# Kernel tuning notes

Measured on AMD Instinct MI355X. Metric: run time of the kernel, lower is better.

The kernel has to match this reference:

```python
import math
import jax, jax.numpy as jnp
import numpy as np

B, T, C = 2, 2048, 1024
N_HEAD, N_KV_HEAD = 16, 4
HEAD_DIM = C // N_HEAD  # 64

def _rope(x, cos, sin):
    # x: (B, T, H, D); cos/sin: (1, T, 1, D//2)
    d = x.shape[3] // 2
    x1, x2 = x[..., :d], x[..., d:]
    return jnp.concatenate([x1 * cos + x2 * sin, -x1 * sin + x2 * cos], axis=3)

def _rms_norm(x):
    return x * jax.lax.rsqrt(jnp.mean(x * x, axis=-1, keepdims=True) + 1e-06)

def setup_inputs() -> dict:
    key = jax.random.key(0)
    ks = jax.random.split(key, 9)
    x = jax.random.normal(ks[0], (B, T, C), dtype=jnp.float32)
    ve = jax.random.normal(ks[1], (B, T, N_KV_HEAD * HEAD_DIM), dtype=jnp.float32)
    cos = jax.random.uniform(ks[2], (1, T, 1, HEAD_DIM // 2), dtype=jnp.float32)
    sin = jax.random.uniform(ks[3], (1, T, 1, HEAD_DIM // 2), dtype=jnp.float32)
    s = 1.0 / math.sqrt(C)
    Wq = jax.random.normal(ks[4], (C, N_HEAD * HEAD_DIM), dtype=jnp.float32) * s
    Wk = jax.random.normal(ks[5], (C, N_KV_HEAD * HEAD_DIM), dtype=jnp.float32) * s
    Wv = jax.random.normal(ks[6], (C, N_KV_HEAD * HEAD_DIM), dtype=jnp.float32) * s
    Wproj = jax.random.normal(ks[7], (C, C), dtype=jnp.float32) * s
    Wg = jax.random.normal(ks[8], (12, N_KV_HEAD), dtype=jnp.float32) * (1.0 / math.sqrt(12))
    return {"x": x, "ve": ve, "cos": cos, "sin": sin,
            "Wq": Wq, "Wk": Wk, "Wv": Wv, "Wproj": Wproj, "Wg": Wg,
            "window_size": 1024}

def reference(x, ve, cos, sin, Wq, Wk, Wv, Wproj, Wg, window_size):
    Bb, Tt, Cc = x.shape
    q = (x @ Wq).reshape(Bb, Tt, N_HEAD, HEAD_DIM)
    k = (x @ Wk).reshape(Bb, Tt, N_KV_HEAD, HEAD_DIM)
    v = (x @ Wv).reshape(Bb, Tt, N_KV_HEAD, HEAD_DIM)
    # value-embedding gate (has_ve layer)
    vee = ve.reshape(Bb, Tt, N_KV_HEAD, HEAD_DIM)
    gate = 3.0 * jax.nn.sigmoid(x[..., :12] @ Wg)  # (B, T, n_kv_head)
    v = v + gate[..., None] * vee
    q = _rope(q, cos, sin)
    k = _rope(k, cos, sin)
    q = _rms_norm(q) * 1.2
    k = _rms_norm(k) * 1.2
    repeats = N_HEAD // N_KV_HEAD
    k = jnp.repeat(k, repeats, axis=2)
    v = jnp.repeat(v, repeats, axis=2)
    # sliding-window causal mask
    row = jnp.arange(Tt)[:, None]
    col = jnp.arange(Tt)[None, :]
    mask = (row >= col) & (row - col <= window_size)
    bias = jnp.where(mask, 0.0, -1e9)  # (T, T)
    scale = 1.0 / math.sqrt(HEAD_DIM)
    scores = jnp.einsum("bqhd,bkhd->bhqk", q, k) * scale + bias[None, None]
    attn = jax.nn.softmax(scores, axis=-1)
    y = jnp.einsum("bhqk,bkhd->bqhd", attn, v).reshape(Bb, Tt, Cc)
    return y @ Wproj
```

## Files before the change

kernel.cpp:

```cpp
#include <hip/hip_runtime.h>


typedef __bf16 bf16x8 __attribute__((ext_vector_type(8)));
typedef __bf16 bf16x4 __attribute__((ext_vector_type(4)));
typedef float  f32x4  __attribute__((ext_vector_type(4)));

__device__ __forceinline__ void g2l16(const __bf16* gp, __bf16* lp) {
  __builtin_amdgcn_global_load_lds(
      (const __attribute__((address_space(1))) unsigned int*)(const void*)gp,
      (__attribute__((address_space(3))) unsigned int*)(void*)lp, 16, 0, 0);
}

__global__ void prep(const float* __restrict__ x, __bf16* __restrict__ xb,
                     float* __restrict__ gate, const float* __restrict__ Wg,
                     const float* __restrict__ Wq, const float* __restrict__ Wk,
                     const float* __restrict__ Wv, const float* __restrict__ Wp,
                     __bf16* __restrict__ Wt, __bf16* __restrict__ Wpt) {
  __shared__ float tile[32][33];
  int bid = blockIdx.x;
  if (bid < 2048) {
    int i = (bid * 256 + threadIdx.x) * 8;
    float4 a = *(const float4*)(x + i);
    float4 b = *(const float4*)(x + i + 4);
    bf16x8 o;
    o[0] = (__bf16)a.x; o[1] = (__bf16)a.y; o[2] = (__bf16)a.z; o[3] = (__bf16)a.w;
    o[4] = (__bf16)b.x; o[5] = (__bf16)b.y; o[6] = (__bf16)b.z; o[7] = (__bf16)b.w;
    *(bf16x8*)(xb + i) = o;
    if (threadIdx.x < 8) {
      int row = bid * 2 + (threadIdx.x >> 2);
      int kvh = threadIdx.x & 3;
      float dot = 0.f;
      for (int j = 0; j < 12; ++j) dot += x[(size_t)row * 1024 + j] * Wg[j * 4 + kvh];
      gate[row * 4 + kvh] = 3.f / (1.f + expf(-dot));
    }
    return;
  }
  bid -= 2048;
  int z = bid >> 10, r = bid & 1023;
  int bx = r & 31, by = r >> 5;
  const float* in; __bf16* out; int Cc;
  if (z == 0)      { in = Wq; out = Wt;               Cc = 1024; }
  else if (z == 1) { in = Wk; out = Wt + 1024 * 1024; Cc = 256; }
  else if (z == 2) { in = Wv; out = Wt + 1280 * 1024; Cc = 256; }
  else             { in = Wp; out = Wpt;              Cc = 1024; }
  int c0 = bx * 32, r0 = by * 32;
  if (c0 >= Cc) return;
  int tx = threadIdx.x & 31, ty = threadIdx.x >> 5;
  for (int i = ty; i < 32; i += 8) tile[i][tx] = in[(size_t)(r0 + i) * Cc + c0 + tx];
  __syncthreads();
  for (int i = ty; i < 32; i += 8) out[(size_t)(c0 + i) * 1024 + r0 + tx] = (__bf16)tile[tx][i];
}

__global__ __launch_bounds__(256) void gemm_qkv(const __bf16* __restrict__ A,
                                                const __bf16* __restrict__ Bt,
                                                const float* __restrict__ cosp,
                                                const float* __restrict__ sinp,
                                                const float* __restrict__ gate,
                                                const float* __restrict__ ve,
                                                __bf16* __restrict__ Qb,
                                                __bf16* __restrict__ Kb,
                                                __bf16* __restrict__ Vt) {
  const int K = 1024;
  __shared__ __bf16 As[2 * 64 * 32];
  __shared__ __bf16 Bs[2 * 128 * 32];
  int tid = threadIdx.x;
  int m0 = blockIdx.x * 64, n0 = blockIdx.y * 128;
  int w = tid >> 6, lane = tid & 63, quad = lane >> 4, l16 = lane & 15;
  int wm = (w >> 1) * 32, wn = (w & 1) * 64;

  f32x4 zero = {0.f, 0.f, 0.f, 0.f};
  f32x4 acc[2][4];
  for (int i = 0; i < 2; ++i) for (int j = 0; j < 4; ++j) acc[i][j] = zero;

  int rsub = lane >> 2, cc = (lane & 3) * 8;
  const __bf16* gA  = A  + (size_t)(m0 + w * 16 + rsub) * K + cc;
  const __bf16* gB0 = Bt + (size_t)(n0 + (2 * w) * 16 + rsub) * K + cc;
  const __bf16* gB1 = Bt + (size_t)(n0 + (2 * w + 1) * 16 + rsub) * K + cc;
  __bf16* lA0  = &As[w * 512];            __bf16* lA1  = &As[2048 + w * 512];
  __bf16* lB00 = &Bs[(2 * w) * 512];      __bf16* lB01 = &Bs[4096 + (2 * w) * 512];
  __bf16* lB10 = &Bs[(2 * w + 1) * 512];  __bf16* lB11 = &Bs[4096 + (2 * w + 1) * 512];

  for (int k0 = 0; k0 < K; k0 += 64) {
    __syncthreads();
    g2l16(gA + k0, lA0);       g2l16(gA + k0 + 32, lA1);
    g2l16(gB0 + k0, lB00);     g2l16(gB0 + k0 + 32, lB01);
    g2l16(gB1 + k0, lB10);     g2l16(gB1 + k0 + 32, lB11);
    __syncthreads();
    for (int ks = 0; ks < 2; ++ks) {
      bf16x8 af[2], bfr[4];
      for (int i = 0; i < 2; ++i)
        af[i] = *(const bf16x8*)(&As[ks * 2048 + (wm + i * 16 + l16) * 32 + quad * 8]);
      for (int j = 0; j < 4; ++j)
        bfr[j] = *(const bf16x8*)(&Bs[ks * 4096 + (wn + j * 16 + l16) * 32 + quad * 8]);
      for (int i = 0; i < 2; ++i)
        for (int j = 0; j < 4; ++j)
          acc[i][j] = __builtin_amdgcn_mfma_f32_16x16x32_bf16(af[i], bfr[j], acc[i][j], 0, 0, 0);
    }
  }

  int ncol = n0 + wn;
  if (ncol < 1280) {
    __bf16* dstbase;
    if (ncol < 1024) dstbase = Qb + (size_t)(ncol >> 6) * 2048 * 64;
    else             dstbase = Kb + (size_t)((ncol - 1024) >> 6) * 2048 * 64;
    int nheads = (ncol < 1024) ? 16 : 4;
    for (int i = 0; i < 2; ++i) {
      for (int r = 0; r < 4; ++r) {
        int m = m0 + wm + i * 16 + quad * 4 + r;
        int bb = m >> 11, t = m & 2047;
        float c0 = cosp[t * 32 + l16], c1 = cosp[t * 32 + 16 + l16];
        float s0 = sinp[t * 32 + l16], s1 = sinp[t * 32 + 16 + l16];
        float v0 = acc[i][0][r], v1 = acc[i][1][r], v2 = acc[i][2][r], v3 = acc[i][3][r];
        float r0 = v0 * c0 + v2 * s0;
        float r1 = v1 * c1 + v3 * s1;
        float r2 = v2 * c0 - v0 * s0;
        float r3 = v3 * c1 - v1 * s1;
        float ss = r0 * r0 + r1 * r1 + r2 * r2 + r3 * r3;
        ss += __shfl_xor(ss, 1, 64); ss += __shfl_xor(ss, 2, 64);
        ss += __shfl_xor(ss, 4, 64); ss += __shfl_xor(ss, 8, 64);
        float sc = rsqrtf(ss * (1.f / 64.f) + 1e-6f) * 1.2f;
        __bf16* dst = dstbase + ((size_t)bb * nheads * 2048 + t) * 64;
        dst[l16]      = (__bf16)(r0 * sc);
        dst[16 + l16] = (__bf16)(r1 * sc);
        dst[32 + l16] = (__bf16)(r2 * sc);
        dst[48 + l16] = (__bf16)(r3 * sc);
      }
    }
  } else {
    int kvh = (ncol - 1280) >> 6;
    for (int i = 0; i < 2; ++i) {
      int mbase = m0 + wm + i * 16 + quad * 4;
      int bb = mbase >> 11;
      int t0 = mbase & 2047;
      float g4[4];
      for (int r = 0; r < 4; ++r) g4[r] = gate[(mbase + r) * 4 + kvh];
      for (int j = 0; j < 4; ++j) {
        int d = j * 16 + l16;
        bf16x4 pk;
        for (int r = 0; r < 4; ++r)
          pk[r] = (__bf16)(acc[i][j][r] + g4[r] * ve[(size_t)(mbase + r) * 256 + kvh * 64 + d]);
        *(bf16x4*)(Vt + ((size_t)(bb * 4 + kvh) * 64 + d) * 2048 + t0) = pk;
      }
    }
  }
}

__global__ __launch_bounds__(512) void attn_kernel(
    const __bf16* __restrict__ Q, const __bf16* __restrict__ K,
    const __bf16* __restrict__ Vt, __bf16* __restrict__ Y,
    const int* __restrict__ winp) {
  const int T = 2048, D = 64, NH = 16, NKV = 4;
  int fid = blockIdx.x + 16 * blockIdx.y + 256 * blockIdx.z;
  int g8 = fid & 7, j = fid >> 3;
  int b = g8 >> 2, kvh = g8 & 3;
  int h = kvh * 4 + (j & 3);
  int qb = (15 - (j >> 2)) * 128;
  int tid = threadIdx.x, w = tid >> 6, lane = tid & 63, quad = lane >> 4, l16 = lane & 15;
  int window = *winp;
  int qw = qb + w * 16;

  __shared__ __bf16 Ks[64 * 72];
  __shared__ __bf16 Vs[64 * 72];

  const __bf16* Qbase = Q + ((size_t)(b * NH + h)) * T * D;
  bf16x8 qf0 = *(const bf16x8*)(Qbase + (size_t)(qw + l16) * D + quad * 8);
  bf16x8 qf1 = *(const bf16x8*)(Qbase + (size_t)(qw + l16) * D + quad * 8 + 32);

  const __bf16* Kbase = K  + ((size_t)(b * NKV + kvh)) * T * D;
  const __bf16* Vbase = Vt + ((size_t)(b * NKV + kvh)) * D * T;

  float lsum = 0.f;
  f32x4 zero = {0.f, 0.f, 0.f, 0.f};
  f32x4 o[4] = {zero, zero, zero, zero};

  int kw = qb - window;
  int kstart = (kw > 0) ? (kw & ~63) : 0;
  int kend = qb + 128;
  const float c1 = 0.125f * 1.44269504f;
  const float c2 = 12.0f * 1.44269504f;
  int q = qw + l16;

  int sr = tid >> 3, sc8 = (tid & 7) * 8;
  bf16x8 kr = *(const bf16x8*)(Kbase + (size_t)(kstart + sr) * D + sc8);
  bf16x8 vr = *(const bf16x8*)(Vbase + (size_t)sr * T + kstart + sc8);

  for (int kt = kstart; kt < kend; kt += 64) {
    __syncthreads();
    *(bf16x8*)(&Ks[sr * 72 + sc8]) = kr;
    *(bf16x8*)(&Vs[sr * 72 + sc8]) = vr;
    __syncthreads();
    int ktn = kt + 64;
    if (ktn < kend) {
      kr = *(const bf16x8*)(Kbase + (size_t)(ktn + sr) * D + sc8);
      vr = *(const bf16x8*)(Vbase + (size_t)sr * T + ktn + sc8);
    }
    if (kt > qw + 15 || kt + 63 < qw - window) continue;
    bool clean = (kt + 63 <= qw) && (qw + 15 - kt <= window);

    for (int g = 0; g < 2; ++g) {
      int kb = g * 32;
      bf16x8 ka0 = *(const bf16x8*)(&Ks[(kb + l16) * 72 + quad * 8]);
      bf16x8 ka1 = *(const bf16x8*)(&Ks[(kb + l16) * 72 + quad * 8 + 32]);
      f32x4 sA = __builtin_amdgcn_mfma_f32_16x16x32_bf16(ka0, qf0, zero, 0, 0, 0);
      sA       = __builtin_amdgcn_mfma_f32_16x16x32_bf16(ka1, qf1, sA, 0, 0, 0);
      bf16x8 kb0 = *(const bf16x8*)(&Ks[(kb + 16 + l16) * 72 + quad * 8]);
      bf16x8 kb1 = *(const bf16x8*)(&Ks[(kb + 16 + l16) * 72 + quad * 8 + 32]);
      f32x4 sB = __builtin_amdgcn_mfma_f32_16x16x32_bf16(kb0, qf0, zero, 0, 0, 0);
      sB       = __builtin_amdgcn_mfma_f32_16x16x32_bf16(kb1, qf1, sB, 0, 0, 0);

      bf16x8 pf;
      if (clean) {
        for (int r = 0; r < 4; ++r) {
          float pA = __builtin_amdgcn_exp2f(sA[r] * c1 - c2);
          float pB = __builtin_amdgcn_exp2f(sB[r] * c1 - c2);
          lsum += pA + pB;
          pf[r] = (__bf16)pA; pf[4 + r] = (__bf16)pB;
        }
      } else {
        for (int r = 0; r < 4; ++r) {
          int kiA = kt + kb + quad * 4 + r;
          int kiB = kiA + 16;
          bool okA = (kiA <= q) && (q - kiA <= window);
          bool okB = (kiB <= q) && (q - kiB <= window);
          float pA = okA ? __builtin_amdgcn_exp2f(sA[r] * c1 - c2) : 0.f;
          float pB = okB ? __builtin_amdgcn_exp2f(sB[r] * c1 - c2) : 0.f;
          lsum += pA + pB;
          pf[r] = (__bf16)pA; pf[4 + r] = (__bf16)pB;
        }
      }
      for (int dc = 0; dc < 4; ++dc) {
        bf16x4 va = *(const bf16x4*)(&Vs[(dc * 16 + l16) * 72 + kb + quad * 4]);
        bf16x4 vb = *(const bf16x4*)(&Vs[(dc * 16 + l16) * 72 + kb + 16 + quad * 4]);
        bf16x8 vf;
        vf[0] = va[0]; vf[1] = va[1]; vf[2] = va[2]; vf[3] = va[3];
        vf[4] = vb[0]; vf[5] = vb[1]; vf[6] = vb[2]; vf[7] = vb[3];
        o[dc] = __builtin_amdgcn_mfma_f32_16x16x32_bf16(vf, pf, o[dc], 0, 0, 0);
      }
    }
  }

  float l = lsum;
  l += __shfl_xor(l, 16, 64);
  l += __shfl_xor(l, 32, 64);
  float inv = 1.f / l;
  size_t base = ((size_t)(b * T + q)) * 1024 + h * 64 + quad * 4;
  for (int dc = 0; dc < 4; ++dc) {
    bf16x4 pk;
    pk[0] = (__bf16)(o[dc][0] * inv); pk[1] = (__bf16)(o[dc][1] * inv);
    pk[2] = (__bf16)(o[dc][2] * inv); pk[3] = (__bf16)(o[dc][3] * inv);
    *(bf16x4*)(Y + base + dc * 16) = pk;
  }
}

__global__ __launch_bounds__(256) void gemm_proj(const __bf16* __restrict__ A,
                                                 const __bf16* __restrict__ Bt,
                                                 float* __restrict__ C,
                                                 int M, int N, int K) {
  __shared__ __bf16 As[2 * 64 * 32];
  __shared__ __bf16 Bs[2 * 128 * 32];
  int tid = threadIdx.x;
  int m0 = blockIdx.x * 64, n0 = blockIdx.y * 128;
  int w = tid >> 6, lane = tid & 63, quad = lane >> 4, l16 = lane & 15;
  int wm = (w >> 1) * 32, wn = (w & 1) * 64;

  f32x4 zero = {0.f, 0.f, 0.f, 0.f};
  f32x4 acc[2][4];
  for (int i = 0; i < 2; ++i) for (int j = 0; j < 4; ++j) acc[i][j] = zero;

  int rsub = lane >> 2, cc = (lane & 3) * 8;
  const __bf16* gA  = A  + (size_t)(m0 + w * 16 + rsub) * K + cc;
  const __bf16* gB0 = Bt + (size_t)(n0 + (2 * w) * 16 + rsub) * K + cc;
  const __bf16* gB1 = Bt + (size_t)(n0 + (2 * w + 1) * 16 + rsub) * K + cc;
  __bf16* lA0  = &As[w * 512];            __bf16* lA1  = &As[2048 + w * 512];
  __bf16* lB00 = &Bs[(2 * w) * 512];      __bf16* lB01 = &Bs[4096 + (2 * w) * 512];
  __bf16* lB10 = &Bs[(2 * w + 1) * 512];  __bf16* lB11 = &Bs[4096 + (2 * w + 1) * 512];

  for (int k0 = 0; k0 < K; k0 += 64) {
    __syncthreads();
    g2l16(gA + k0, lA0);       g2l16(gA + k0 + 32, lA1);
    g2l16(gB0 + k0, lB00);     g2l16(gB0 + k0 + 32, lB01);
    g2l16(gB1 + k0, lB10);     g2l16(gB1 + k0 + 32, lB11);
    __syncthreads();
    for (int ks = 0; ks < 2; ++ks) {
      bf16x8 af[2], bfr[4];
      for (int i = 0; i < 2; ++i)
        af[i] = *(const bf16x8*)(&As[ks * 2048 + (wm + i * 16 + l16) * 32 + quad * 8]);
      for (int j = 0; j < 4; ++j)
        bfr[j] = *(const bf16x8*)(&Bs[ks * 4096 + (wn + j * 16 + l16) * 32 + quad * 8]);
      for (int i = 0; i < 2; ++i)
        for (int j = 0; j < 4; ++j)
          acc[i][j] = __builtin_amdgcn_mfma_f32_16x16x32_bf16(af[i], bfr[j], acc[i][j], 0, 0, 0);
    }
  }
  for (int i = 0; i < 2; ++i)
    for (int j = 0; j < 4; ++j)
      for (int r = 0; r < 4; ++r)
        C[(size_t)(m0 + wm + i * 16 + quad * 4 + r) * N + n0 + wn + j * 16 + l16] = acc[i][j][r];
}

extern "C" void kernel_launch(void* const* d_in, const int* in_sizes, int n_in,
                              void* d_out, int out_size, void* d_ws, size_t ws_size,
                              hipStream_t stream) {
  const float* x     = (const float*)d_in[0];
  const float* ve    = (const float*)d_in[1];
  const float* cosp  = (const float*)d_in[2];
  const float* sinp  = (const float*)d_in[3];
  const float* Wq    = (const float*)d_in[4];
  const float* Wk    = (const float*)d_in[5];
  const float* Wv    = (const float*)d_in[6];
  const float* Wproj = (const float*)d_in[7];
  const float* Wg    = (const float*)d_in[8];
  const int*   win   = (const int*)d_in[9];
  float* out = (float*)d_out;

  char* ws = (char*)d_ws;
  __bf16* xb   = (__bf16*)(ws);
  __bf16* Wt   = (__bf16*)(ws + 8388608);
  __bf16* Wpt  = (__bf16*)(ws + 11534336);
  float*  gate = (float*)(ws + 13631488);
  __bf16* Qb   = (__bf16*)(ws + 13697024);
  __bf16* Kb   = (__bf16*)(ws + 22085632);
  __bf16* Vt   = (__bf16*)(ws + 24182784);
  __bf16* Y    = (__bf16*)(ws + 26279936);

  prep<<<2048 + 4096, 256, 0, stream>>>(x, xb, gate, Wg, Wq, Wk, Wv, Wproj, Wt, Wpt);
  gemm_qkv<<<dim3(64, 12), 256, 0, stream>>>(xb, Wt, cosp, sinp, gate, ve, Qb, Kb, Vt);
  attn_kernel<<<dim3(16, 16, 2), 512, 0, stream>>>(Qb, Kb, Vt, Y, win);
  gemm_proj<<<dim3(64, 8), 256, 0, stream>>>(Y, Wpt, out, 4096, 1024, 1024);
}
```

Measured before the change: 163.5 us.

## Split attention key range into two partitions and combine partial results

Splits each query block's key range into two halves handled by separate workgroups, doubling the attention grid to 1024 blocks. Each part writes unnormalized fp32 outputs and row sums, and a new combine kernel adds the two parts, normalizes and writes bf16 Y. The fixed-max softmax (constant offset) lets the parts be summed without rescaling. The aim is better CU occupancy and balance, at the cost of extra fp32 traffic (about 33 MB written and read) and an additional kernel launch.

After: 172.8 us. 5.7% more time.

```diff
diff --git a/kernel.cpp b/kernel.cpp
--- a/kernel.cpp
+++ b/kernel.cpp
@@ -145,16 +145,16 @@
   }
 }
 
-__global__ __launch_bounds__(512) void attn_kernel(
+__global__ __launch_bounds__(512) void attn_part(
     const __bf16* __restrict__ Q, const __bf16* __restrict__ K,
-    const __bf16* __restrict__ Vt, __bf16* __restrict__ Y,
+    const __bf16* __restrict__ Vt, float* __restrict__ Op, float* __restrict__ Lp,
     const int* __restrict__ winp) {
   const int T = 2048, D = 64, NH = 16, NKV = 4;
-  int fid = blockIdx.x + 16 * blockIdx.y + 256 * blockIdx.z;
-  int g8 = fid & 7, j = fid >> 3;
-  int b = g8 >> 2, kvh = g8 & 3;
+  int fid = blockIdx.x + 16 * blockIdx.y;
+  int kvh = fid & 3, j = fid >> 2;
   int h = kvh * 4 + (j & 3);
   int qb = (15 - (j >> 2)) * 128;
+  int s = blockIdx.z >> 1, b = blockIdx.z & 1;
   int tid = threadIdx.x, w = tid >> 6, lane = tid & 63, quad = lane >> 4, l16 = lane & 15;
   int window = *winp;
   int qw = qb + w * 16;
@@ -174,8 +174,12 @@
   f32x4 o[4] = {zero, zero, zero, zero};
 
   int kw = qb - window;
-  int kstart = (kw > 0) ? (kw & ~63) : 0;
-  int kend = qb + 128;
+  int kfull = (kw > 0) ? (kw & ~63) : 0;
+  int kendf = qb + 128;
+  int half = ((kendf - kfull) >> 6) >> 1;
+  int mid = kfull + (half << 6);
+  int kstart = s ? mid : kfull;
+  int kend   = s ? kendf : mid;
   const float c1 = 0.125f * 1.44269504f;
   const float c2 = 12.0f * 1.44269504f;
   int q = qw + l16;
@@ -242,14 +246,31 @@
   float l = lsum;
   l += __shfl_xor(l, 16, 64);
   l += __shfl_xor(l, 32, 64);
-  float inv = 1.f / l;
-  size_t base = ((size_t)(b * T + q)) * 1024 + h * 64 + quad * 4;
-  for (int dc = 0; dc < 4; ++dc) {
-    bf16x4 pk;
-    pk[0] = (__bf16)(o[dc][0] * inv); pk[1] = (__bf16)(o[dc][1] * inv);
-    pk[2] = (__bf16)(o[dc][2] * inv); pk[3] = (__bf16)(o[dc][3] * inv);
-    *(bf16x4*)(Y + base + dc * 16) = pk;
-  }
+  size_t rowi = ((size_t)((s * 2 + b) * NH + h)) * T + q;
+  if (quad == 0) Lp[rowi] = l;
+  float* ob = Op + rowi * 64;
+  for (int dc = 0; dc < 4; ++dc)
+    *(f32x4*)(ob + dc * 16 + quad * 4) = o[dc];
+}
+
+__global__ __launch_bounds__(256) void combine(const float* __restrict__ Op,
+                                               const float* __restrict__ Lp,
+                                               __bf16* __restrict__ Y) {
+  int idx = blockIdx.x * 256 + threadIdx.x;
+  int i8 = idx * 8;
+  int row = i8 >> 6, d = i8 & 63;
+  const float* p0 = Op + (size_t)row * 64 + d;
+  const float* p1 = p0 + (size_t)65536 * 64;
+  float inv = 1.f / (Lp[row] + Lp[row + 65536]);
+  float4 a0 = *(const float4*)(p0), a1 = *(const float4*)(p0 + 4);
+  float4 b0 = *(const float4*)(p1), b1 = *(const float4*)(p1 + 4);
+  bf16x8 o;
+  o[0] = (__bf16)((a0.x + b0.x) * inv); o[1] = (__bf16)((a0.y + b0.y) * inv);
+  o[2] = (__bf16)((a0.z + b0.z) * inv); o[3] = (__bf16)((a0.w + b0.w) * inv);
+  o[4] = (__bf16)((a1.x + b1.x) * inv); o[5] = (__bf16)((a1.y + b1.y) * inv);
+  o[6] = (__bf16)((a1.z + b1.z) * inv); o[7] = (__bf16)((a1.w + b1.w) * inv);
+  int bb = row >> 15, hh = (row >> 11) & 15, qq = row & 2047;
+  *(bf16x8*)(Y + ((size_t)(bb * 2048 + qq) * 1024) + hh * 64 + d) = o;
 }
 
 __global__ __launch_bounds__(256) void gemm_proj(const __bf16* __restrict__ A,
@@ -322,9 +343,12 @@
   __bf16* Kb   = (__bf16*)(ws + 22085632);
   __bf16* Vt   = (__bf16*)(ws + 24182784);
   __bf16* Y    = (__bf16*)(ws + 26279936);
+  float*  Op   = (float*)(ws + 34668544);
+  float*  Lp   = (float*)(ws + 68222976);
 
   prep<<<2048 + 4096, 256, 0, stream>>>(x, xb, gate, Wg, Wq, Wk, Wv, Wproj, Wt, Wpt);
   gemm_qkv<<<dim3(64, 12), 256, 0, stream>>>(xb, Wt, cosp, sinp, gate, ve, Qb, Kb, Vt);
-  attn_kernel<<<dim3(16, 16, 2), 512, 0, stream>>>(Qb, Kb, Vt, Y, win);
+  attn_part<<<dim3(16, 16, 4), 512, 0, stream>>>(Qb, Kb, Vt, Op, Lp, win);
+  combine<<<2048, 256, 0, stream>>>(Op, Lp, Y);
   gemm_proj<<<dim3(64, 8), 256, 0, stream>>>(Y, Wpt, out, 4096, 1024, 1024);
 }
```
